# Kernel optimization log

Hardware: AMD Instinct MI355X
Metric: run time of the kernel (lower is better)

## Reference

```python
import jax, jax.numpy as jnp
import numpy as np

B, F = 1048576, 128


def setup_inputs() -> dict:
    key = jax.random.key(0)
    ks = jax.random.split(key, 16)
    def w(k, shape):
        return jax.random.normal(k, shape, dtype=jnp.float32) * 0.1
    x = jax.random.uniform(ks[0], (B, F), dtype=jnp.float32, minval=0.05, maxval=1.0)
    return {
        "x": x,
        "W_prod": w(ks[1], (F, 1)), "b_prod": w(ks[2], (1,)),
        "W_sum": w(ks[3], (F + 1, 1)), "b_sum": w(ks[4], (1,)),
        "w_dln": w(ks[5], (1, 1)), "W_ln": w(ks[6], (2, 1)),
        "w_dsin": w(ks[7], (1, 1)), "W_sin": w(ks[8], (2, 1)),
        "w_dcos": w(ks[9], (1, 1)), "W_cos": w(ks[10], (2, 1)),
        "w_de": w(ks[11], (1, 1)), "W_e": w(ks[12], (2, 1)),
        "w_dtanh": w(ks[13], (1, 1)), "W_tanh": w(ks[14], (2, 1)),
    }


def _stage(h, fn, w_drop, W):
    # h: [B,1]. Drop = Dense(1, relu, no bias) on fn(h); then Dense(2->1, no bias)
    d = jax.nn.relu(fn(h) * w_drop[0, 0])          # [B,1]
    return jnp.concatenate([d, h], axis=-1) @ W    # [B,1]


def reference(x, W_prod, b_prod, W_sum, b_sum,
              w_dln, W_ln, w_dsin, W_sin, w_dcos, W_cos,
              w_de, W_e, w_dtanh, W_tanh):
    # ProductBlock: exp(Dense(log(abs(x))))  -> product-of-powers via log-space
    x_prod = jnp.exp(jnp.log(jnp.abs(x)) @ W_prod + b_prod)          # [B,1]
    # SumBlock over [x, x_prod]
    x_sum = jnp.concatenate([x, x_prod], axis=-1) @ W_sum + b_sum    # [B,1]
    x_ln = _stage(x_sum, lambda t: jnp.log(jnp.abs(t)), w_dln, W_ln)
    x_sin = _stage(x_ln, jnp.sin, w_dsin, W_sin)
    x_cos = _stage(x_sin, jnp.cos, w_dcos, W_cos)
    x_e = _stage(x_cos, jnp.exp, w_de, W_e)
    x_tanh = _stage(x_e, jnp.tanh, w_dtanh, W_tanh)
    return x_tanh
```

## Files before the change

### kernel.cpp

```cpp
#include <hip/hip_runtime.h>


__global__ __launch_bounds__(256) void funcblock_kernel(
    const float* __restrict__ x,
    const float* __restrict__ W_prod, const float* __restrict__ b_prod,
    const float* __restrict__ W_sum,  const float* __restrict__ b_sum,
    const float* __restrict__ w_dln,  const float* __restrict__ W_ln,
    const float* __restrict__ w_dsin, const float* __restrict__ W_sin,
    const float* __restrict__ w_dcos, const float* __restrict__ W_cos,
    const float* __restrict__ w_de,   const float* __restrict__ W_e,
    const float* __restrict__ w_dtanh,const float* __restrict__ W_tanh,
    float* __restrict__ out, int B)
{
    __shared__ float pbuf[4][64];
    __shared__ float sbuf[4][64];

    const int tid  = threadIdx.x;
    const int lane = tid & 63;
    const int wid  = tid >> 6;
    const int u    = lane & 7;
    const int g    = lane >> 3;

    float4 wp[4], ws[4];
    #pragma unroll
    for (int j = 0; j < 4; ++j) {
        wp[j] = reinterpret_cast<const float4*>(W_prod)[u + 8 * j];
        ws[j] = reinterpret_cast<const float4*>(W_sum)[u + 8 * j];
    }
    const float ws128 = W_sum[128];
    const float bp2 = b_prod[0] * 1.44269504088896340736f;
    const float bs = b_sum[0];
    const float wdln  = w_dln[0],  wln0  = W_ln[0],  wln1  = W_ln[1];
    const float wdsin = w_dsin[0], wsin0 = W_sin[0], wsin1 = W_sin[1];
    const float wdcos = w_dcos[0], wcos0 = W_cos[0], wcos1 = W_cos[1];
    const float wde   = w_de[0],   we0   = W_e[0],   we1   = W_e[1];
    const float wdtanh= w_dtanh[0],wt0   = W_tanh[0],wt1   = W_tanh[1];

    const int rows_per_block = 256;
    for (int base = blockIdx.x * rows_per_block; base < B;
         base += gridDim.x * rows_per_block) {
        const int wbase = base + wid * 64;

        #pragma unroll 2
        for (int it = 0; it < 8; ++it) {
            const int row = wbase + it * 8 + g;
            float p = 0.0f, s = 0.0f;
            if (row < B) {
                const float4* xr =
                    reinterpret_cast<const float4*>(x + (size_t)row * 128);
                float4 xv[4];
                #pragma unroll
                for (int j = 0; j < 4; ++j) xv[j] = xr[u + 8 * j];
                #pragma unroll
                for (int j = 0; j < 4; ++j) {
                    p += __log2f(__builtin_fabsf(xv[j].x)) * wp[j].x;
                    p += __log2f(__builtin_fabsf(xv[j].y)) * wp[j].y;
                    p += __log2f(__builtin_fabsf(xv[j].z)) * wp[j].z;
                    p += __log2f(__builtin_fabsf(xv[j].w)) * wp[j].w;
                    s += xv[j].x * ws[j].x + xv[j].y * ws[j].y
                       + xv[j].z * ws[j].z + xv[j].w * ws[j].w;
                }
            }
            #pragma unroll
            for (int m = 4; m >= 1; m >>= 1) {
                p += __shfl_xor(p, m, 64);
                s += __shfl_xor(s, m, 64);
            }
            if (u == 0) {
                pbuf[wid][it * 8 + g] = p;
                sbuf[wid][it * 8 + g] = s;
            }
        }
        __syncthreads();

        const int row = wbase + lane;
        const float p = pbuf[wid][lane];
        const float s = sbuf[wid][lane];
        __syncthreads();

        const float x_prod = __builtin_amdgcn_exp2f(p + bp2);
        float h = s + x_prod * ws128 + bs;
        float d;
        d = fmaxf(logf(fabsf(h)) * wdln, 0.0f);  h = d * wln0  + h * wln1;
        d = fmaxf(sinf(h) * wdsin, 0.0f);        h = d * wsin0 + h * wsin1;
        d = fmaxf(cosf(h) * wdcos, 0.0f);        h = d * wcos0 + h * wcos1;
        d = fmaxf(expf(h) * wde,   0.0f);        h = d * we0   + h * we1;
        d = fmaxf(tanhf(h) * wdtanh, 0.0f);      h = d * wt0   + h * wt1;
        if (row < B) out[row] = h;
    }
}

extern "C" void kernel_launch(void* const* d_in, const int* in_sizes, int n_in,
                              void* d_out, int out_size, void* d_ws, size_t ws_size,
                              hipStream_t stream) {
    const float* x      = (const float*)d_in[0];
    const float* W_prod = (const float*)d_in[1];
    const float* b_prod = (const float*)d_in[2];
    const float* W_sum  = (const float*)d_in[3];
    const float* b_sum  = (const float*)d_in[4];
    const float* w_dln  = (const float*)d_in[5];
    const float* W_ln   = (const float*)d_in[6];
    const float* w_dsin = (const float*)d_in[7];
    const float* W_sin  = (const float*)d_in[8];
    const float* w_dcos = (const float*)d_in[9];
    const float* W_cos  = (const float*)d_in[10];
    const float* w_de   = (const float*)d_in[11];
    const float* W_e    = (const float*)d_in[12];
    const float* w_dtanh= (const float*)d_in[13];
    const float* W_tanh = (const float*)d_in[14];
    float* out = (float*)d_out;

    const int B = out_size;
    const int block = 256;
    const int grid  = 2048;

    hipLaunchKernelGGL(funcblock_kernel, dim3(grid), dim3(block), 0, stream,
                       x, W_prod, b_prod, W_sum, b_sum,
                       w_dln, W_ln, w_dsin, W_sin, w_dcos, W_cos,
                       w_de, W_e, w_dtanh, W_tanh, out, B);
}
```

Baseline: 100.8 us.

## Replace shared-memory row transposition with wave shuffles and one-shot grid

Drops the LDS buffers and both block-wide barriers. The per-row partial sums are now broadcast across each wavefront with shuffles, and each lane picks out its own row's value. The grid-stride loop is replaced by one block per 256 rows (grid sized from B), and the inner loop unroll is raised to 4. This removes barrier stalls and LDS traffic in exchange for extra shuffles per iteration and many more launched blocks, each of which reloads the weights.

```diff
diff --git a/kernel.cpp b/kernel.cpp
--- a/kernel.cpp
+++ b/kernel.cpp
@@ -12,9 +12,6 @@
     const float* __restrict__ w_dtanh,const float* __restrict__ W_tanh,
     float* __restrict__ out, int B)
 {
-    __shared__ float pbuf[4][64];
-    __shared__ float sbuf[4][64];
-
     const int tid  = threadIdx.x;
     const int lane = tid & 63;
     const int wid  = tid >> 6;
@@ -36,58 +33,49 @@
     const float wde   = w_de[0],   we0   = W_e[0],   we1   = W_e[1];
     const float wdtanh= w_dtanh[0],wt0   = W_tanh[0],wt1   = W_tanh[1];
 
-    const int rows_per_block = 256;
-    for (int base = blockIdx.x * rows_per_block; base < B;
-         base += gridDim.x * rows_per_block) {
-        const int wbase = base + wid * 64;
+    const int wbase = (blockIdx.x * 4 + wid) * 64;
 
-        #pragma unroll 2
-        for (int it = 0; it < 8; ++it) {
-            const int row = wbase + it * 8 + g;
-            float p = 0.0f, s = 0.0f;
-            if (row < B) {
-                const float4* xr =
-                    reinterpret_cast<const float4*>(x + (size_t)row * 128);
-                float4 xv[4];
-                #pragma unroll
-                for (int j = 0; j < 4; ++j) xv[j] = xr[u + 8 * j];
-                #pragma unroll
-                for (int j = 0; j < 4; ++j) {
-                    p += __log2f(__builtin_fabsf(xv[j].x)) * wp[j].x;
-                    p += __log2f(__builtin_fabsf(xv[j].y)) * wp[j].y;
-                    p += __log2f(__builtin_fabsf(xv[j].z)) * wp[j].z;
-                    p += __log2f(__builtin_fabsf(xv[j].w)) * wp[j].w;
-                    s += xv[j].x * ws[j].x + xv[j].y * ws[j].y
-                       + xv[j].z * ws[j].z + xv[j].w * ws[j].w;
-                }
-            }
+    float pr = 0.0f, sr = 0.0f;
+    #pragma unroll 4
+    for (int it = 0; it < 8; ++it) {
+        const int row = wbase + it * 8 + g;
+        float p = 0.0f, s = 0.0f;
+        if (row < B) {
+            const float4* xr =
+                reinterpret_cast<const float4*>(x + (size_t)row * 128);
+            float4 xv[4];
             #pragma unroll
-            for (int m = 4; m >= 1; m >>= 1) {
-                p += __shfl_xor(p, m, 64);
-                s += __shfl_xor(s, m, 64);
-            }
-            if (u == 0) {
-                pbuf[wid][it * 8 + g] = p;
-                sbuf[wid][it * 8 + g] = s;
+            for (int j = 0; j < 4; ++j) xv[j] = xr[u + 8 * j];
+            #pragma unroll
+            for (int j = 0; j < 4; ++j) {
+                p += __log2f(__builtin_fabsf(xv[j].x)) * wp[j].x;
+                p += __log2f(__builtin_fabsf(xv[j].y)) * wp[j].y;
+                p += __log2f(__builtin_fabsf(xv[j].z)) * wp[j].z;
+                p += __log2f(__builtin_fabsf(xv[j].w)) * wp[j].w;
+                s += xv[j].x * ws[j].x + xv[j].y * ws[j].y
+                   + xv[j].z * ws[j].z + xv[j].w * ws[j].w;
             }
         }
-        __syncthreads();
+        #pragma unroll
+        for (int m = 4; m >= 1; m >>= 1) {
+            p += __shfl_xor(p, m, 64);
+            s += __shfl_xor(s, m, 64);
+        }
+        const float pb = __shfl(p, (lane & 7) * 8, 64);
+        const float sb = __shfl(s, (lane & 7) * 8, 64);
+        if (g == it) { pr = pb; sr = sb; }
+    }
 
-        const int row = wbase + lane;
-        const float p = pbuf[wid][lane];
-        const float s = sbuf[wid][lane];
-        __syncthreads();
-
-        const float x_prod = __builtin_amdgcn_exp2f(p + bp2);
-        float h = s + x_prod * ws128 + bs;
-        float d;
-        d = fmaxf(logf(fabsf(h)) * wdln, 0.0f);  h = d * wln0  + h * wln1;
-        d = fmaxf(sinf(h) * wdsin, 0.0f);        h = d * wsin0 + h * wsin1;
-        d = fmaxf(cosf(h) * wdcos, 0.0f);        h = d * wcos0 + h * wcos1;
-        d = fmaxf(expf(h) * wde,   0.0f);        h = d * we0   + h * we1;
-        d = fmaxf(tanhf(h) * wdtanh, 0.0f);      h = d * wt0   + h * wt1;
-        if (row < B) out[row] = h;
-    }
+    const float x_prod = __builtin_amdgcn_exp2f(pr + bp2);
+    float h = sr + x_prod * ws128 + bs;
+    float d;
+    d = fmaxf(logf(fabsf(h)) * wdln, 0.0f);  h = d * wln0  + h * wln1;
+    d = fmaxf(sinf(h) * wdsin, 0.0f);        h = d * wsin0 + h * wsin1;
+    d = fmaxf(cosf(h) * wdcos, 0.0f);        h = d * wcos0 + h * wcos1;
+    d = fmaxf(expf(h) * wde,   0.0f);        h = d * we0   + h * we1;
+    d = fmaxf(tanhf(h) * wdtanh, 0.0f);      h = d * wt0   + h * wt1;
+    const int orow = wbase + lane;
+    if (orow < B) out[orow] = h;
 }
 
 extern "C" void kernel_launch(void* const* d_in, const int* in_sizes, int n_in,
@@ -112,7 +100,7 @@
 
     const int B = out_size;
     const int block = 256;
-    const int grid  = 2048;
+    const int grid  = (B + 255) / 256;
 
     hipLaunchKernelGGL(funcblock_kernel, dim3(grid), dim3(block), 0, stream,
                        x, W_prod, b_prod, W_sum, b_sum,
```

Measured after the change: 101.5 us. No clear change (+0.7%).
